# Kernel optimization log

Measured on AMD Instinct MI355X. Metric: run time of the kernel, lower is better.

## Reference

```python
import jax, jax.numpy as jnp
import numpy as np

NEG_INF = -1e9


def setup_inputs() -> dict:
    key0 = jax.random.key(0)
    ks = jax.random.split(key0, 7)
    B, Tq, Tv, D, U = 8, 512, 512, 512, 128
    query = jax.random.normal(ks[0], (B, Tq, D), dtype=jnp.float32)
    key = jax.random.normal(ks[1], (B, Tv, D), dtype=jnp.float32)
    value = jax.random.normal(ks[2], (B, Tv, D), dtype=jnp.float32)
    mask = jax.random.randint(ks[3], (B, Tv), 0, 2).astype(bool)
    mask = mask.at[:, 0].set(True)  # ensure no fully-masked row
    Wa = jax.random.normal(ks[4], (D, U), dtype=jnp.float32) * (1.0 / np.sqrt(D))
    Ua = jax.random.normal(ks[5], (D, U), dtype=jnp.float32) * (1.0 / np.sqrt(D))
    scale = jax.random.normal(ks[6], (U,), dtype=jnp.float32) * 0.1
    return {"query": query, "key": key, "value": value, "mask": mask,
            "Wa": Wa, "Ua": Ua, "scale": scale}


def reference(query, key, value, mask, Wa, Ua, scale):
    # Dense projections (no bias)
    q = query @ Wa          # [B, Tq, U]
    k = key @ Ua            # [B, Tv, U]
    # Additive (Bahdanau) scores with learned per-unit scale:
    # scores[b,i,j] = sum_u scale[u] * tanh(q[b,i,u] + k[b,j,u])
    t = jnp.tanh(q[:, :, None, :] + k[:, None, :, :])   # [B, Tq, Tv, U]
    scores = jnp.einsum('bijU,U->bij', t, scale)         # [B, Tq, Tv]
    # Mask padded keys/values then softmax over Tv
    scores = jnp.where(mask[:, None, :], scores, NEG_INF)
    weights = jax.nn.softmax(scores, axis=-1)            # [B, Tq, Tv]
    # Weighted sum of values (query_mask is all-True in source -> no-op)
    context = jnp.einsum('bij,bjd->bid', weights, value) # [B, Tq, D]
    return context
```

## Files before the change

kernel.cpp:

```cpp
#include <hip/hip_runtime.h>

constexpr int Bb = 8;
constexpr int Tq = 512;
constexpr int Tv = 512;
constexpr int Dd = 512;
constexpr int Uu = 128;
constexpr float C2LOG2E = 2.88539008177792681f;
constexpr float LOG2E   = 1.44269504088896341f;

__global__ __launch_bounds__(512) void compact_kernel(
    const int* __restrict__ mask, int* __restrict__ jidx,
    int* __restrict__ posArr, int* __restrict__ cntArr)
{
    const int wv = threadIdx.x >> 6;
    const int ln = threadIdx.x & 63;
#pragma unroll
    for (int c = 0; c < 8; ++c) jidx[wv * 512 + c * 64 + ln] = 0;
    int base = 0;
#pragma unroll
    for (int c = 0; c < 8; ++c) {
        const int j = c * 64 + ln;
        const int v = (mask[wv * 512 + j] != 0);
        const unsigned long long bits = __ballot(v);
        const int pos = base + (int)__popcll(bits & ((1ull << ln) - 1ull));
        if (v) jidx[wv * 512 + pos] = j;
        posArr[wv * 512 + j] = v ? pos : -1;
        base += (int)__popcll(bits);
    }
    if (ln == 0) cntArr[wv] = base;
}

__global__ __launch_bounds__(256) void proj_kernel(
    const float* __restrict__ query,
    const float* __restrict__ key,
    const float* __restrict__ Wa,
    const float* __restrict__ Ua,
    const int* __restrict__ posArr,
    float* __restrict__ qf2, float* __restrict__ kT)
{
    const int R    = blockIdx.x * 16;
    const bool isQ = R < Bb * Tq;
    const float* __restrict__ src = isQ ? query : key;
    const float* __restrict__ W   = isQ ? Wa : Ua;
    const int Rloc = isQ ? R : R - Bb * Tq;

    __shared__ float x[16 * Dd];
    const int t = threadIdx.x;

    {
        const float4* __restrict__ s4 =
            reinterpret_cast<const float4*>(src + (size_t)Rloc * Dd);
        float4* x4 = reinterpret_cast<float4*>(x);
#pragma unroll
        for (int m = 0; m < 8; ++m) x4[t + 256 * m] = s4[t + 256 * m];
    }
    __syncthreads();

    const int ub = t & 63;
    const int rh = t >> 6;
    float acc[4][2] = {{0,0},{0,0},{0,0},{0,0}};

#pragma unroll 2
    for (int d4 = 0; d4 < Dd / 4; ++d4) {
        const int d = d4 * 4;
        const float w0x = W[(d + 0) * Uu + ub],      w1x = W[(d + 0) * Uu + ub + 64];
        const float w0y = W[(d + 1) * Uu + ub],      w1y = W[(d + 1) * Uu + ub + 64];
        const float w0z = W[(d + 2) * Uu + ub],      w1z = W[(d + 2) * Uu + ub + 64];
        const float w0w = W[(d + 3) * Uu + ub],      w1w = W[(d + 3) * Uu + ub + 64];
#pragma unroll
        for (int k = 0; k < 4; ++k) {
            const float4 xv = *reinterpret_cast<const float4*>(x + (rh * 4 + k) * Dd + d);
            acc[k][0] = fmaf(xv.x, w0x, acc[k][0]);
            acc[k][0] = fmaf(xv.y, w0y, acc[k][0]);
            acc[k][0] = fmaf(xv.z, w0z, acc[k][0]);
            acc[k][0] = fmaf(xv.w, w0w, acc[k][0]);
            acc[k][1] = fmaf(xv.x, w1x, acc[k][1]);
            acc[k][1] = fmaf(xv.y, w1y, acc[k][1]);
            acc[k][1] = fmaf(xv.z, w1z, acc[k][1]);
            acc[k][1] = fmaf(xv.w, w1w, acc[k][1]);
        }
    }

    if (isQ) {
#pragma unroll
        for (int k = 0; k < 4; ++k) {
            const size_t row = (size_t)(Rloc + rh * 4 + k);
            qf2[row * Uu + ub]      = C2LOG2E * acc[k][0];
            qf2[row * Uu + ub + 64] = C2LOG2E * acc[k][1];
        }
    } else {
        float* __restrict__ kb = kT + (size_t)(Rloc >> 9) * Uu * Tv;
#pragma unroll
        for (int k = 0; k < 4; ++k) {
            const int row = Rloc + rh * 4 + k;
            const int p   = posArr[row];
            if (p >= 0) {
                kb[(size_t)ub        * Tv + p] = C2LOG2E * acc[k][0];
                kb[(size_t)(ub + 64) * Tv + p] = C2LOG2E * acc[k][1];
            }
        }
    }
}

__global__ __launch_bounds__(512) void attn_kernel(
    const float* __restrict__ qf2, const float* __restrict__ kT,
    const float* __restrict__ value,
    const int* __restrict__ jidx, const int* __restrict__ cntArr,
    const float* __restrict__ scale,
    float* __restrict__ out)
{
    const int r0 = blockIdx.x * 8;
    const int b  = r0 >> 9;
    const int t  = threadIdx.x;

    __shared__ float q2[8 * Uu];
    __shared__ float s2[Uu];
    __shared__ int   jl[Tv];
    __shared__ float w[8 * Tv];
    __shared__ float pbuf[8 * Dd];
    __shared__ float inv8[8];

    const int cnt = cntArr[b];

    jl[t] = jidx[b * Tv + t];
    if (t < 256)
        reinterpret_cast<float4*>(q2)[t] =
            reinterpret_cast<const float4*>(qf2 + (size_t)r0 * Uu)[t];
    else if (t < 384) s2[t - 256] = scale[t - 256];
    __syncthreads();

    const int jc = t;
    if (jc < cnt) {
        const float* __restrict__ kb = kT + (size_t)b * Uu * Tv + jc;
        float acc[8] = {0,0,0,0,0,0,0,0};
#pragma unroll 2
        for (int u4 = 0; u4 < Uu / 4; ++u4) {
            const float kx = kb[(size_t)(u4 * 4 + 0) * Tv];
            const float ky = kb[(size_t)(u4 * 4 + 1) * Tv];
            const float kz = kb[(size_t)(u4 * 4 + 2) * Tv];
            const float kw = kb[(size_t)(u4 * 4 + 3) * Tv];
            const float4 sv = reinterpret_cast<const float4*>(s2)[u4];
#pragma unroll
            for (int i = 0; i < 8; ++i) {
                const float4 qv = *reinterpret_cast<const float4*>(q2 + i * Uu + u4 * 4);
                float e0 = __builtin_amdgcn_exp2f(qv.x + kx);
                float e1 = __builtin_amdgcn_exp2f(qv.y + ky);
                float e2 = __builtin_amdgcn_exp2f(qv.z + kz);
                float e3 = __builtin_amdgcn_exp2f(qv.w + kw);
                acc[i] = fmaf(sv.x, __builtin_amdgcn_rcpf(e0 + 1.f), acc[i]);
                acc[i] = fmaf(sv.y, __builtin_amdgcn_rcpf(e1 + 1.f), acc[i]);
                acc[i] = fmaf(sv.z, __builtin_amdgcn_rcpf(e2 + 1.f), acc[i]);
                acc[i] = fmaf(sv.w, __builtin_amdgcn_rcpf(e3 + 1.f), acc[i]);
            }
        }
#pragma unroll
        for (int i = 0; i < 8; ++i) w[i * Tv + jc] = -2.f * acc[i];
    } else {
#pragma unroll
        for (int i = 0; i < 8; ++i) w[i * Tv + jc] = 0.f;
    }
    __syncthreads();

    {
        const int wv = t >> 6, ln = t & 63;
        float* __restrict__ row = w + wv * Tv;
        float vals[8];
        float m = -3e38f;
#pragma unroll
        for (int c = 0; c < 8; ++c) {
            const int e = ln + 64 * c;
            vals[c] = (e < cnt) ? row[e] : -3e38f;
            m = fmaxf(m, vals[c]);
        }
#pragma unroll
        for (int off = 32; off; off >>= 1) m = fmaxf(m, __shfl_xor(m, off, 64));
        float sum = 0.f;
#pragma unroll
        for (int c = 0; c < 8; ++c) {
            const int e = ln + 64 * c;
            if (e < cnt) {
                float ex = __builtin_amdgcn_exp2f((vals[c] - m) * LOG2E);
                row[e] = ex;
                sum += ex;
            }
        }
#pragma unroll
        for (int off = 32; off; off >>= 1) sum += __shfl_xor(sum, off, 64);
        if (ln == 0) inv8[wv] = 1.0f / sum;
    }
    __syncthreads();

    const int cntp = (cnt + 3) & ~3;
    const int mid  = ((cntp >> 1) + 3) & ~3;
    const int g  = t >> 8;
    const int c  = t & 255;
    const int d0 = c * 2;
    const int jbeg = g ? mid : 0;
    const int jend = g ? cntp : mid;
    const float* __restrict__ vb = value + (size_t)b * Tv * Dd + d0;
    float ax[8], ay[8];
#pragma unroll
    for (int i = 0; i < 8; ++i) { ax[i] = 0.f; ay[i] = 0.f; }

    for (int jj = jbeg; jj < jend; jj += 4) {
        const int4 rows = *reinterpret_cast<const int4*>(jl + jj);
        const float2 v0 = *reinterpret_cast<const float2*>(vb + (size_t)rows.x * Dd);
        const float2 v1 = *reinterpret_cast<const float2*>(vb + (size_t)rows.y * Dd);
        const float2 v2 = *reinterpret_cast<const float2*>(vb + (size_t)rows.z * Dd);
        const float2 v3 = *reinterpret_cast<const float2*>(vb + (size_t)rows.w * Dd);
#pragma unroll
        for (int i = 0; i < 8; ++i) {
            const float4 wq = *reinterpret_cast<const float4*>(w + i * Tv + jj);
            ax[i] = fmaf(wq.x, v0.x, ax[i]); ay[i] = fmaf(wq.x, v0.y, ay[i]);
            ax[i] = fmaf(wq.y, v1.x, ax[i]); ay[i] = fmaf(wq.y, v1.y, ay[i]);
            ax[i] = fmaf(wq.z, v2.x, ax[i]); ay[i] = fmaf(wq.z, v2.y, ay[i]);
            ax[i] = fmaf(wq.w, v3.x, ax[i]); ay[i] = fmaf(wq.w, v3.y, ay[i]);
        }
    }

    if (g == 1) {
#pragma unroll
        for (int i = 0; i < 8; ++i) {
            float2 p; p.x = ax[i]; p.y = ay[i];
            *reinterpret_cast<float2*>(pbuf + i * Dd + d0) = p;
        }
    }
    __syncthreads();
    if (g == 0) {
#pragma unroll
        for (int i = 0; i < 8; ++i) {
            const float inv = inv8[i];
            const float2 p1 = *reinterpret_cast<const float2*>(pbuf + i * Dd + d0);
            float2 o;
            o.x = (ax[i] + p1.x) * inv;
            o.y = (ay[i] + p1.y) * inv;
            *reinterpret_cast<float2*>(out + (size_t)(r0 + i) * Dd + d0) = o;
        }
    }
}

extern "C" void kernel_launch(void* const* d_in, const int* in_sizes, int n_in,
                              void* d_out, int out_size, void* d_ws, size_t ws_size,
                              hipStream_t stream)
{
    const float* query = (const float*)d_in[0];
    const float* key   = (const float*)d_in[1];
    const float* value = (const float*)d_in[2];
    const int*   mask  = (const int*)d_in[3];
    const float* Wa    = (const float*)d_in[4];
    const float* Ua    = (const float*)d_in[5];
    const float* scale = (const float*)d_in[6];
    float* out = (float*)d_out;

    float* qf2   = (float*)d_ws;
    float* kT    = qf2 + Bb * Tq * Uu;
    int* jidxW   = (int*)(kT + Bb * Uu * Tv);
    int* posArr  = jidxW + Bb * Tv;
    int* cntArr  = posArr + Bb * Tv;

    compact_kernel<<<1, 512, 0, stream>>>(mask, jidxW, posArr, cntArr);
    proj_kernel<<<(2 * Bb * Tq) / 16, 256, 0, stream>>>(query, key, Wa, Ua, posArr, qf2, kT);
    attn_kernel<<<(Bb * Tq) / 8, 512, 0, stream>>>(qf2, kT, value, jidxW, cntArr, scale, out);
}
```

Baseline: 169.1 us.

## Fuse mask compaction into consumer kernels and split score work over unit halves

Drops the separate single-block compaction kernel: proj_kernel recomputes compacted positions for its 16 key rows, and attn_kernel rebuilds the index list per block with ballots. The score phase now divides the 128 units between two thread halves, so all 512 threads work even when fewer keys survive the mask, and the halves are combined through shared memory. This removes one launch and its serialization, and keeps threads busy that previously sat idle on masked-out keys. The cost is redundant mask scans in every block and extra barriers in a loop.

```diff
diff --git a/kernel.cpp b/kernel.cpp
--- a/kernel.cpp
+++ b/kernel.cpp
@@ -8,34 +8,12 @@
 constexpr float C2LOG2E = 2.88539008177792681f;
 constexpr float LOG2E   = 1.44269504088896341f;
 
-__global__ __launch_bounds__(512) void compact_kernel(
-    const int* __restrict__ mask, int* __restrict__ jidx,
-    int* __restrict__ posArr, int* __restrict__ cntArr)
-{
-    const int wv = threadIdx.x >> 6;
-    const int ln = threadIdx.x & 63;
-#pragma unroll
-    for (int c = 0; c < 8; ++c) jidx[wv * 512 + c * 64 + ln] = 0;
-    int base = 0;
-#pragma unroll
-    for (int c = 0; c < 8; ++c) {
-        const int j = c * 64 + ln;
-        const int v = (mask[wv * 512 + j] != 0);
-        const unsigned long long bits = __ballot(v);
-        const int pos = base + (int)__popcll(bits & ((1ull << ln) - 1ull));
-        if (v) jidx[wv * 512 + pos] = j;
-        posArr[wv * 512 + j] = v ? pos : -1;
-        base += (int)__popcll(bits);
-    }
-    if (ln == 0) cntArr[wv] = base;
-}
-
 __global__ __launch_bounds__(256) void proj_kernel(
     const float* __restrict__ query,
     const float* __restrict__ key,
     const float* __restrict__ Wa,
     const float* __restrict__ Ua,
-    const int* __restrict__ posArr,
+    const int* __restrict__ mask,
     float* __restrict__ qf2, float* __restrict__ kT)
 {
     const int R    = blockIdx.x * 16;
@@ -45,6 +23,7 @@
     const int Rloc = isQ ? R : R - Bb * Tq;
 
     __shared__ float x[16 * Dd];
+    __shared__ int posLoc[16];
     const int t = threadIdx.x;
 
     {
@@ -53,6 +32,20 @@
         float4* x4 = reinterpret_cast<float4*>(x);
 #pragma unroll
         for (int m = 0; m < 8; ++m) x4[t + 256 * m] = s4[t + 256 * m];
+    }
+    if (!isQ && t < 64) {
+        const int b  = Rloc >> 9;
+        const int j0 = Rloc & 511;
+        int base = 0;
+#pragma unroll
+        for (int c = 0; c < 8; ++c) {
+            const int j = c * 64 + t;
+            const int v = (mask[b * 512 + j] != 0);
+            const unsigned long long bits = __ballot(v);
+            const int pos = base + (int)__popcll(bits & ((1ull << t) - 1ull));
+            if (j >= j0 && j < j0 + 16) posLoc[j - j0] = v ? pos : -1;
+            base += (int)__popcll(bits);
+        }
     }
     __syncthreads();
 
@@ -92,8 +85,7 @@
         float* __restrict__ kb = kT + (size_t)(Rloc >> 9) * Uu * Tv;
 #pragma unroll
         for (int k = 0; k < 4; ++k) {
-            const int row = Rloc + rh * 4 + k;
-            const int p   = posArr[row];
+            const int p = posLoc[rh * 4 + k];
             if (p >= 0) {
                 kb[(size_t)ub        * Tv + p] = C2LOG2E * acc[k][0];
                 kb[(size_t)(ub + 64) * Tv + p] = C2LOG2E * acc[k][1];
@@ -105,7 +97,7 @@
 __global__ __launch_bounds__(512) void attn_kernel(
     const float* __restrict__ qf2, const float* __restrict__ kT,
     const float* __restrict__ value,
-    const int* __restrict__ jidx, const int* __restrict__ cntArr,
+    const int* __restrict__ mask,
     const float* __restrict__ scale,
     float* __restrict__ out)
 {
@@ -117,49 +109,81 @@
     __shared__ float s2[Uu];
     __shared__ int   jl[Tv];
     __shared__ float w[8 * Tv];
-    __shared__ float pbuf[8 * Dd];
+    __shared__ float pbuf[8 * Tv];
     __shared__ float inv8[8];
-
-    const int cnt = cntArr[b];
-
-    jl[t] = jidx[b * Tv + t];
+    __shared__ int   cntS;
+
+    jl[t] = 0;
     if (t < 256)
         reinterpret_cast<float4*>(q2)[t] =
             reinterpret_cast<const float4*>(qf2 + (size_t)r0 * Uu)[t];
     else if (t < 384) s2[t - 256] = scale[t - 256];
     __syncthreads();
-
-    const int jc = t;
-    if (jc < cnt) {
-        const float* __restrict__ kb = kT + (size_t)b * Uu * Tv + jc;
+    if (t < 64) {
+        int base = 0;
+#pragma unroll
+        for (int c = 0; c < 8; ++c) {
+            const int j = c * 64 + t;
+            const int v = (mask[b * 512 + j] != 0);
+            const unsigned long long bits = __ballot(v);
+            const int pos = base + (int)__popcll(bits & ((1ull << t) - 1ull));
+            if (v) jl[pos] = j;
+            base += (int)__popcll(bits);
+        }
+        if (t == 0) cntS = base;
+    }
+    __syncthreads();
+
+    const int cnt   = cntS;
+    const int cntp4 = (cnt + 3) & ~3;
+
+    const int s  = t & 255;
+    const int uh = t >> 8;
+    const int u4b = uh * 16;
+    const int niter = (cntp4 + 255) >> 8;
+    for (int it = 0; it < niter; ++it) {
+        const int jc = s + it * 256;
         float acc[8] = {0,0,0,0,0,0,0,0};
+        if (jc < cnt) {
+            const float* __restrict__ kb = kT + (size_t)b * Uu * Tv + jc;
 #pragma unroll 2
-        for (int u4 = 0; u4 < Uu / 4; ++u4) {
-            const float kx = kb[(size_t)(u4 * 4 + 0) * Tv];
-            const float ky = kb[(size_t)(u4 * 4 + 1) * Tv];
-            const float kz = kb[(size_t)(u4 * 4 + 2) * Tv];
-            const float kw = kb[(size_t)(u4 * 4 + 3) * Tv];
-            const float4 sv = reinterpret_cast<const float4*>(s2)[u4];
-#pragma unroll
-            for (int i = 0; i < 8; ++i) {
-                const float4 qv = *reinterpret_cast<const float4*>(q2 + i * Uu + u4 * 4);
-                float e0 = __builtin_amdgcn_exp2f(qv.x + kx);
-                float e1 = __builtin_amdgcn_exp2f(qv.y + ky);
-                float e2 = __builtin_amdgcn_exp2f(qv.z + kz);
-                float e3 = __builtin_amdgcn_exp2f(qv.w + kw);
-                acc[i] = fmaf(sv.x, __builtin_amdgcn_rcpf(e0 + 1.f), acc[i]);
-                acc[i] = fmaf(sv.y, __builtin_amdgcn_rcpf(e1 + 1.f), acc[i]);
-                acc[i] = fmaf(sv.z, __builtin_amdgcn_rcpf(e2 + 1.f), acc[i]);
-                acc[i] = fmaf(sv.w, __builtin_amdgcn_rcpf(e3 + 1.f), acc[i]);
-            }
-        }
-#pragma unroll
-        for (int i = 0; i < 8; ++i) w[i * Tv + jc] = -2.f * acc[i];
-    } else {
-#pragma unroll
-        for (int i = 0; i < 8; ++i) w[i * Tv + jc] = 0.f;
-    }
-    __syncthreads();
+            for (int u4 = u4b; u4 < u4b + 16; ++u4) {
+                const float kx = kb[(size_t)(u4 * 4 + 0) * Tv];
+                const float ky = kb[(size_t)(u4 * 4 + 1) * Tv];
+                const float kz = kb[(size_t)(u4 * 4 + 2) * Tv];
+                const float kw = kb[(size_t)(u4 * 4 + 3) * Tv];
+                const float4 sv = reinterpret_cast<const float4*>(s2)[u4];
+#pragma unroll
+                for (int i = 0; i < 8; ++i) {
+                    const float4 qv = *reinterpret_cast<const float4*>(q2 + i * Uu + u4 * 4);
+                    float e0 = __builtin_amdgcn_exp2f(qv.x + kx);
+                    float e1 = __builtin_amdgcn_exp2f(qv.y + ky);
+                    float e2 = __builtin_amdgcn_exp2f(qv.z + kz);
+                    float e3 = __builtin_amdgcn_exp2f(qv.w + kw);
+                    acc[i] = fmaf(sv.x, __builtin_amdgcn_rcpf(e0 + 1.f), acc[i]);
+                    acc[i] = fmaf(sv.y, __builtin_amdgcn_rcpf(e1 + 1.f), acc[i]);
+                    acc[i] = fmaf(sv.z, __builtin_amdgcn_rcpf(e2 + 1.f), acc[i]);
+                    acc[i] = fmaf(sv.w, __builtin_amdgcn_rcpf(e3 + 1.f), acc[i]);
+                }
+            }
+        }
+        if (uh == 1 && jc < cnt) {
+#pragma unroll
+            for (int i = 0; i < 8; ++i) pbuf[i * Tv + jc] = acc[i];
+        }
+        __syncthreads();
+        if (uh == 0 && jc < cntp4) {
+            if (jc < cnt) {
+#pragma unroll
+                for (int i = 0; i < 8; ++i)
+                    w[i * Tv + jc] = -2.f * (acc[i] + pbuf[i * Tv + jc]);
+            } else {
+#pragma unroll
+                for (int i = 0; i < 8; ++i) w[i * Tv + jc] = 0.f;
+            }
+        }
+        __syncthreads();
+    }
 
     {
         const int wv = t >> 6, ln = t & 63;
@@ -190,13 +214,12 @@
     }
     __syncthreads();
 
-    const int cntp = (cnt + 3) & ~3;
-    const int mid  = ((cntp >> 1) + 3) & ~3;
+    const int mid  = ((cntp4 >> 1) + 3) & ~3;
     const int g  = t >> 8;
     const int c  = t & 255;
     const int d0 = c * 2;
     const int jbeg = g ? mid : 0;
-    const int jend = g ? cntp : mid;
+    const int jend = g ? cntp4 : mid;
     const float* __restrict__ vb = value + (size_t)b * Tv * Dd + d0;
     float ax[8], ay[8];
 #pragma unroll
@@ -218,11 +241,12 @@
         }
     }
 
+    __syncthreads();
     if (g == 1) {
 #pragma unroll
         for (int i = 0; i < 8; ++i) {
             float2 p; p.x = ax[i]; p.y = ay[i];
-            *reinterpret_cast<float2*>(pbuf + i * Dd + d0) = p;
+            *reinterpret_cast<float2*>(pbuf + i * Tv + d0) = p;
         }
     }
     __syncthreads();
@@ -230,7 +254,7 @@
 #pragma unroll
         for (int i = 0; i < 8; ++i) {
             const float inv = inv8[i];
-            const float2 p1 = *reinterpret_cast<const float2*>(pbuf + i * Dd + d0);
+            const float2 p1 = *reinterpret_cast<const float2*>(pbuf + i * Tv + d0);
             float2 o;
             o.x = (ax[i] + p1.x) * inv;
             o.y = (ay[i] + p1.y) * inv;
@@ -252,13 +276,9 @@
     const float* scale = (const float*)d_in[6];
     float* out = (float*)d_out;
 
-    float* qf2   = (float*)d_ws;
-    float* kT    = qf2 + Bb * Tq * Uu;
-    int* jidxW   = (int*)(kT + Bb * Uu * Tv);
-    int* posArr  = jidxW + Bb * Tv;
-    int* cntArr  = posArr + Bb * Tv;
-
-    compact_kernel<<<1, 512, 0, stream>>>(mask, jidxW, posArr, cntArr);
-    proj_kernel<<<(2 * Bb * Tq) / 16, 256, 0, stream>>>(query, key, Wa, Ua, posArr, qf2, kT);
-    attn_kernel<<<(Bb * Tq) / 8, 512, 0, stream>>>(qf2, kT, value, jidxW, cntArr, scale, out);
+    float* qf2 = (float*)d_ws;
+    float* kT  = qf2 + Bb * Tq * Uu;
+
+    proj_kernel<<<(2 * Bb * Tq) / 16, 256, 0, stream>>>(query, key, Wa, Ua, mask, qf2, kT);
+    attn_kernel<<<(Bb * Tq) / 8, 512, 0, stream>>>(qf2, kT, value, mask, scale, out);
 }
```

After: 178.9 us. 5.8% more time.
